# Kernel tuning notes

Hardware: AMD Instinct MI355X
Metric: run time of the kernel (lower is better)

## Reference

```python
import jax, jax.numpy as jnp
import numpy as np

# Dims: B walkers, NELEC electrons split equally into NSPIN=2 spins of NE each,
# D backflow feature dim, NION ions, SPATIAL=3 spatial dims, NORB orbitals/spin.
B, NELEC, D, NION, SPATIAL, NORB = 1024, 64, 32, 16, 3, 32
NSPIN = 2
NE = NELEC // NSPIN


def setup_inputs() -> dict:
    key = jax.random.key(0)
    ks = jax.random.split(key, 6)
    x = jax.random.normal(ks[0], (B, NELEC, D), jnp.float32)
    r_ei = jax.random.normal(ks[1], (B, NELEC, NION, SPATIAL), jnp.float32)
    # per-spin Dense(norbitals) on concatenated pair features [y_p, y_i] (2D -> NORB)
    W_orb = jax.random.normal(ks[2], (NSPIN, 2 * D, NORB), jnp.float32) / np.sqrt(2 * D)
    b_orb = jax.random.normal(ks[3], (NSPIN, NORB), jnp.float32) * 0.01
    # anisotropic decay: a 3x3 matrix per (spin, ion, orbital)
    W_env_dim = jax.random.normal(ks[4], (NSPIN, NION, SPATIAL, NORB, SPATIAL), jnp.float32) / np.sqrt(SPATIAL)
    # linear combination over ions (Dense(1), no bias)
    w_env_ion = jax.random.normal(ks[5], (NSPIN, NION), jnp.float32) / np.sqrt(NION)
    return dict(x=x, r_ei=r_ei, W_orb=W_orb, b_orb=b_orb,
                W_env_dim=W_env_dim, w_env_ion=w_env_ion)


def reference(x, r_ei, W_orb, b_orb, W_env_dim, w_env_ion):
    # Equal spin split -> stack spins as a leading axis (s = NSPIN)
    xs = jnp.stack(jnp.split(x, NSPIN, axis=-2), axis=0)       # (s, B, NE, D)
    res = jnp.stack(jnp.split(r_ei, NSPIN, axis=-3), axis=0)   # (s, B, NE, NION, 3)

    # Pairwise doubly-equivariant inputs: pair[p, i] = concat(y_p, y_i)
    xp = jnp.broadcast_to(xs[:, :, :, None, :], (NSPIN, B, NE, NE, D))
    xi = jnp.broadcast_to(xs[:, :, None, :, :], (NSPIN, B, NE, NE, D))
    pair = jnp.concatenate([xp, xi], axis=-1)                  # (s, B, NE, NE, 2D)
    orbs = jnp.einsum('sbpif,sfo->sbpio', pair, W_orb) + b_orb[:, None, None, None, :]

    # Anisotropic exponential envelope: exp(-||A_{ion,orb} (r - R_ion)||), combined over ions
    scale = jnp.einsum('sbnid,sidoe->sbnoie', res, W_env_dim)  # (s, B, NE, NORB, NION, 3)
    dist = jnp.linalg.norm(scale, axis=-1)                     # (s, B, NE, NORB, NION)
    env = jnp.einsum('sbnoi,si->sbno', jnp.exp(-dist), w_env_ion)  # (s, B, NE, NORB)

    # envelope depends on electron i (axis -2 of orbs), broadcast over p (axis -3)
    return orbs * env[:, :, None, :, :]                        # (s, B, NE, NE, NORB)
```

## Files before the change

### kernel.cpp

```cpp
#include <hip/hip_runtime.h>

#define BATCH 1024
#define NELEC 64
#define DF    32
#define NION  16
#define NORB  32
#define NE    32
#define NSB   2048
#define FACT_FLOATS (NSB * NE * NORB)
#define M_PAD 8192
#define WS_NEEDED ((size_t)(M_PAD + 3 * FACT_FLOATS) * 4)

__global__ __launch_bounds__(256) void k0_gram(
    const float* __restrict__ W_env,
    float* __restrict__ Mg)
{
    int id = blockIdx.x * 256 + threadIdx.x;
    if (id >= 2 * NION * NORB) return;
    int s = id >> 9, rem = id & 511, i = rem >> 5, o = rem & 31;
    const float* base = W_env + ((size_t)((s*NION + i) * 3) * NORB + o) * 3;
    float a0[3], a1[3], a2[3];
    #pragma unroll
    for (int e = 0; e < 3; ++e) {
        a0[e] = base[e];
        a1[e] = base[96 + e];
        a2[e] = base[192 + e];
    }
    float* out = Mg + ((size_t)(s*NION + i) * 6) * NORB + o;
    out[0*NORB] = a0[0]*a0[0] + a0[1]*a0[1] + a0[2]*a0[2];
    out[1*NORB] = a1[0]*a1[0] + a1[1]*a1[1] + a1[2]*a1[2];
    out[2*NORB] = a2[0]*a2[0] + a2[1]*a2[1] + a2[2]*a2[2];
    out[3*NORB] = 2.f*(a0[0]*a1[0] + a0[1]*a1[1] + a0[2]*a1[2]);
    out[4*NORB] = 2.f*(a0[0]*a2[0] + a0[1]*a2[1] + a0[2]*a2[2]);
    out[5*NORB] = 2.f*(a1[0]*a2[0] + a1[1]*a2[1] + a1[2]*a2[2]);
}

__global__ __launch_bounds__(256) void k1_factors(
    const float* __restrict__ x,
    const float* __restrict__ r_ei,
    const float* __restrict__ W_orb,
    const float* __restrict__ b_orb,
    const float* __restrict__ w_ion,
    const float* __restrict__ Mg,
    float* __restrict__ Uf, float* __restrict__ Ef, float* __restrict__ Wf)
{
    __shared__ float sworb[2*DF*NORB];
    __shared__ float sM[NION*6*NORB];
    __shared__ float sr[NE*52];
    __shared__ float swion[NION];

    const int t   = threadIdx.x;
    const int blk = blockIdx.x;
    const int s   = blk >> 10;
    const int b   = blk & (BATCH - 1);

    {
        const float4* g = (const float4*)(W_orb + (size_t)s * 2*DF*NORB);
        float4* d = (float4*)sworb;
        d[t] = g[t]; d[t + 256] = g[t + 256];
    }
    {
        const float4* g = (const float4*)(Mg + (size_t)s * NION*6*NORB);
        float4* d = (float4*)sM;
        d[t] = g[t]; d[t + 256] = g[t + 256]; d[t + 512] = g[t + 512];
    }
    if (t < 128) {
        const int row = t >> 2, seg = t & 3;
        const float4* g = (const float4*)(r_ei + ((size_t)b*NELEC + s*NE + row) * NION * 3);
        float4* d = (float4*)(sr + row*52 + seg*12);
        d[0] = g[seg*3 + 0]; d[1] = g[seg*3 + 1]; d[2] = g[seg*3 + 2];
    }
    if (t < NION) swion[t] = w_ion[s*NION + t];
    __syncthreads();

    const int n  = t >> 3;
    const int o0 = (t & 7) * 4;

    float u[4] = {0,0,0,0}, v[4] = {0,0,0,0};
    const float* xrow = x + ((size_t)b*NELEC + s*NE + n) * DF;
    #pragma unroll
    for (int db = 0; db < 8; ++db) {
        const float4 xa = *(const float4*)(xrow + db*4);
        #pragma unroll
        for (int k = 0; k < 4; ++k) {
            const int d = db*4 + k;
            const float4 w0 = *(const float4*)(sworb + d*NORB + o0);
            const float4 w1 = *(const float4*)(sworb + (DF + d)*NORB + o0);
            const float xk = (&xa.x)[k];
            u[0] += xk*w0.x; u[1] += xk*w0.y; u[2] += xk*w0.z; u[3] += xk*w0.w;
            v[0] += xk*w1.x; v[1] += xk*w1.y; v[2] += xk*w1.z; v[3] += xk*w1.w;
        }
    }

    float e[4] = {0,0,0,0};
    #pragma unroll
    for (int i = 0; i < NION; ++i) {
        const float r0 = sr[n*52 + i*3 + 0];
        const float r1 = sr[n*52 + i*3 + 1];
        const float r2 = sr[n*52 + i*3 + 2];
        const float q00 = r0*r0, q11 = r1*r1, q22 = r2*r2;
        const float q01 = r0*r1, q02 = r0*r2, q12 = r1*r2;
        const float* mp = sM + (size_t)(i*6) * NORB + o0;
        float d2[4];
        {
            const float4 m = *(const float4*)(mp + 0*NORB);
            d2[0] = m.x*q00; d2[1] = m.y*q00; d2[2] = m.z*q00; d2[3] = m.w*q00;
        }
        {
            const float4 m = *(const float4*)(mp + 1*NORB);
            d2[0] += m.x*q11; d2[1] += m.y*q11; d2[2] += m.z*q11; d2[3] += m.w*q11;
        }
        {
            const float4 m = *(const float4*)(mp + 2*NORB);
            d2[0] += m.x*q22; d2[1] += m.y*q22; d2[2] += m.z*q22; d2[3] += m.w*q22;
        }
        {
            const float4 m = *(const float4*)(mp + 3*NORB);
            d2[0] += m.x*q01; d2[1] += m.y*q01; d2[2] += m.z*q01; d2[3] += m.w*q01;
        }
        {
            const float4 m = *(const float4*)(mp + 4*NORB);
            d2[0] += m.x*q02; d2[1] += m.y*q02; d2[2] += m.z*q02; d2[3] += m.w*q02;
        }
        {
            const float4 m = *(const float4*)(mp + 5*NORB);
            d2[0] += m.x*q12; d2[1] += m.y*q12; d2[2] += m.z*q12; d2[3] += m.w*q12;
        }
        const float wi = swion[i];
        #pragma unroll
        for (int j = 0; j < 4; ++j) {
            const float dd = fmaxf(d2[j], 0.f);
            e[j] += wi * __expf(-sqrtf(dd));
        }
    }

    const float4 bq = *(const float4*)(b_orb + s*NORB + o0);
    const size_t wbase = (size_t)blk * (NE*NORB) + (size_t)t * 4;
    float4 uo, eo, wo;
    uo.x = u[0]; uo.y = u[1]; uo.z = u[2]; uo.w = u[3];
    eo.x = e[0]; eo.y = e[1]; eo.z = e[2]; eo.w = e[3];
    wo.x = (v[0] + bq.x) * e[0];
    wo.y = (v[1] + bq.y) * e[1];
    wo.z = (v[2] + bq.z) * e[2];
    wo.w = (v[3] + bq.w) * e[3];
    *(float4*)(Uf + wbase) = uo;
    *(float4*)(Ef + wbase) = eo;
    *(float4*)(Wf + wbase) = wo;
}

__global__ __launch_bounds__(256) void k2_expand(
    const float* __restrict__ Uf,
    const float* __restrict__ Ef,
    const float* __restrict__ Wf,
    float* __restrict__ out)
{
    __shared__ float sU[NE][NORB];
    const int t   = threadIdx.x;
    const int blk = blockIdx.x;
    const size_t base = (size_t)blk * (NE*NORB);

    ((float4*)&sU[0][0])[t] = ((const float4*)(Uf + base))[t];
    const float4 e4 = ((const float4*)(Ef + base))[t];
    const float4 w4 = ((const float4*)(Wf + base))[t];
    __syncthreads();

    const int o0 = (t & 7) * 4;
    float4* outp = (float4*)(out + (size_t)blk * (NE*NE*NORB));
    #pragma unroll
    for (int p = 0; p < NE; ++p) {
        const float4 u4 = *(const float4*)&sU[p][o0];
        float4 r;
        r.x = u4.x*e4.x + w4.x;
        r.y = u4.y*e4.y + w4.y;
        r.z = u4.z*e4.z + w4.z;
        r.w = u4.w*e4.w + w4.w;
        outp[p*256 + t] = r;
    }
}

__global__ __launch_bounds__(256) void deq_orbital_fused(
    const float* __restrict__ x, const float* __restrict__ r_ei,
    const float* __restrict__ W_orb, const float* __restrict__ b_orb,
    const float* __restrict__ W_env, const float* __restrict__ w_ion,
    float* __restrict__ out)
{
    __shared__ float sx[NE][DF];
    __shared__ float sworb[2*DF][NORB];
    __shared__ float sr[NE][NION*3];
    __shared__ float swe[NION*3*NORB*3];
    __shared__ float sU[NE][NORB];
    __shared__ float sV[NE][NORB];
    __shared__ float sE[NE][NORB];
    __shared__ float sb[NORB];
    __shared__ float swion[NION];

    const int t   = threadIdx.x;
    const int blk = blockIdx.x;
    const int s   = blk >> 10;
    const int b   = blk & (BATCH - 1);

    {
        const float4* xg = (const float4*)(x + (size_t)(b*NELEC + s*NE) * DF);
        ((float4*)&sx[0][0])[t] = xg[t];
    }
    {
        const float4* wg = (const float4*)(W_orb + (size_t)s * 2*DF*NORB);
        float4* d = (float4*)&sworb[0][0];
        d[t] = wg[t]; d[t + 256] = wg[t + 256];
    }
    {
        const float4* rg = (const float4*)(r_ei + (size_t)(b*NELEC + s*NE) * NION * 3);
        float4* d = (float4*)&sr[0][0];
        d[t] = rg[t];
        if (t < 128) d[t + 256] = rg[t + 256];
    }
    {
        const float4* weg = (const float4*)(W_env + (size_t)s * NION*3*NORB*3);
        float4* d = (float4*)swe;
        for (int j = t; j < 1152; j += 256) d[j] = weg[j];
    }
    if (t < NORB) sb[t]    = b_orb[s*NORB + t];
    if (t < NION) swion[t] = w_ion[s*NION + t];
    __syncthreads();

    const int o  = t & 31;
    const int ng = t >> 5;
    float u_acc[4], v_acc[4];
    #pragma unroll
    for (int uu = 0; uu < 4; ++uu) { u_acc[uu] = 0.f; v_acc[uu] = 0.f; }
    #pragma unroll
    for (int d = 0; d < DF; ++d) {
        const float w0 = sworb[d][o];
        const float w1 = sworb[DF + d][o];
        #pragma unroll
        for (int uu = 0; uu < 4; ++uu) {
            const float xv = sx[ng*4 + uu][d];
            u_acc[uu] += xv * w0;
            v_acc[uu] += xv * w1;
        }
    }
    #pragma unroll
    for (int uu = 0; uu < 4; ++uu) {
        sU[ng*4 + uu][o] = u_acc[uu];
        sV[ng*4 + uu][o] = v_acc[uu];
    }
    #pragma unroll
    for (int uu = 0; uu < 4; ++uu) {
        const int nn = ng*4 + uu;
        float acc = 0.f;
        #pragma unroll
        for (int i = 0; i < NION; ++i) {
            const float r0 = sr[nn][i*3 + 0];
            const float r1 = sr[nn][i*3 + 1];
            const float r2 = sr[nn][i*3 + 2];
            const float* wp = &swe[i*3*NORB*3 + o*3];
            const float s0 = r0*wp[0] + r1*wp[NORB*3    ] + r2*wp[2*NORB*3    ];
            const float s1 = r0*wp[1] + r1*wp[NORB*3 + 1] + r2*wp[2*NORB*3 + 1];
            const float s2 = r0*wp[2] + r1*wp[NORB*3 + 2] + r2*wp[2*NORB*3 + 2];
            const float dist = sqrtf(s0*s0 + s1*s1 + s2*s2);
            acc += __expf(-dist) * swion[i];
        }
        sE[nn][o] = acc;
        sV[nn][o] = (v_acc[uu] + sb[o]) * acc;
    }
    __syncthreads();

    const int io = t >> 3;
    const int o0 = (t & 7) * 4;
    const float4 e4 = *(const float4*)&sE[io][o0];
    const float4 w4 = *(const float4*)&sV[io][o0];
    float4* outp = (float4*)(out + (size_t)blk * (NE*NE*NORB));
    #pragma unroll
    for (int p = 0; p < NE; ++p) {
        const float4 u4 = *(const float4*)&sU[p][o0];
        float4 r;
        r.x = u4.x*e4.x + w4.x;
        r.y = u4.y*e4.y + w4.y;
        r.z = u4.z*e4.z + w4.z;
        r.w = u4.w*e4.w + w4.w;
        outp[p*256 + t] = r;
    }
}

extern "C" void kernel_launch(void* const* d_in, const int* in_sizes, int n_in,
                              void* d_out, int out_size, void* d_ws, size_t ws_size,
                              hipStream_t stream) {
    const float* x     = (const float*)d_in[0];
    const float* r_ei  = (const float*)d_in[1];
    const float* W_orb = (const float*)d_in[2];
    const float* b_orb = (const float*)d_in[3];
    const float* W_env = (const float*)d_in[4];
    const float* w_ion = (const float*)d_in[5];
    float* out = (float*)d_out;

    if (ws_size >= WS_NEEDED) {
        float* Mg = (float*)d_ws;
        float* Uf = Mg + M_PAD;
        float* Ef = Uf + FACT_FLOATS;
        float* Wf = Ef + FACT_FLOATS;
        k0_gram<<<4, 256, 0, stream>>>(W_env, Mg);
        k1_factors<<<NSB, 256, 0, stream>>>(x, r_ei, W_orb, b_orb, w_ion, Mg,
                                            Uf, Ef, Wf);
        k2_expand<<<NSB, 256, 0, stream>>>(Uf, Ef, Wf, out);
    } else {
        deq_orbital_fused<<<NSB, 256, 0, stream>>>(x, r_ei, W_orb, b_orb,
                                                   W_env, w_ion, out);
    }
}
```

Measured before the change: 93.22 us.

## Remap k1 threads to one orbital by four electrons and drop r_ei staging

Changes the k1_factors thread mapping from one electron by four orbitals to one orbital by four electrons. Weight and Gram-matrix reads from shared memory become scalar, conflict-free and reused across four electrons, while x and r_ei are read straight from global memory as wavefront-uniform broadcast loads. The r_ei shared staging buffer is removed. In exchange, stores become scalar rather than float4 and the r_ei loads rely on the scalar or global cache.

```diff
diff --git a/kernel.cpp b/kernel.cpp
--- a/kernel.cpp
+++ b/kernel.cpp
@@ -46,7 +46,6 @@
 {
     __shared__ float sworb[2*DF*NORB];
     __shared__ float sM[NION*6*NORB];
-    __shared__ float sr[NE*52];
     __shared__ float swion[NION];
 
     const int t   = threadIdx.x;
@@ -64,88 +63,69 @@
         float4* d = (float4*)sM;
         d[t] = g[t]; d[t + 256] = g[t + 256]; d[t + 512] = g[t + 512];
     }
-    if (t < 128) {
-        const int row = t >> 2, seg = t & 3;
-        const float4* g = (const float4*)(r_ei + ((size_t)b*NELEC + s*NE + row) * NION * 3);
-        float4* d = (float4*)(sr + row*52 + seg*12);
-        d[0] = g[seg*3 + 0]; d[1] = g[seg*3 + 1]; d[2] = g[seg*3 + 2];
-    }
     if (t < NION) swion[t] = w_ion[s*NION + t];
     __syncthreads();
 
-    const int n  = t >> 3;
-    const int o0 = (t & 7) * 4;
+    const int o  = t & 31;
+    const int ng = t >> 5;
+    const int n0 = ng * 4;
+
+    const size_t erow = (size_t)b*NELEC + s*NE + n0;
+    const float* xrow = x    + erow * DF;
+    const float* rrow = r_ei + erow * (NION*3);
 
     float u[4] = {0,0,0,0}, v[4] = {0,0,0,0};
-    const float* xrow = x + ((size_t)b*NELEC + s*NE + n) * DF;
-    #pragma unroll
+    #pragma unroll 2
     for (int db = 0; db < 8; ++db) {
-        const float4 xa = *(const float4*)(xrow + db*4);
+        float4 xa[4];
+        #pragma unroll
+        for (int e = 0; e < 4; ++e)
+            xa[e] = *(const float4*)(xrow + e*DF + db*4);
         #pragma unroll
         for (int k = 0; k < 4; ++k) {
             const int d = db*4 + k;
-            const float4 w0 = *(const float4*)(sworb + d*NORB + o0);
-            const float4 w1 = *(const float4*)(sworb + (DF + d)*NORB + o0);
-            const float xk = (&xa.x)[k];
-            u[0] += xk*w0.x; u[1] += xk*w0.y; u[2] += xk*w0.z; u[3] += xk*w0.w;
-            v[0] += xk*w1.x; v[1] += xk*w1.y; v[2] += xk*w1.z; v[3] += xk*w1.w;
-        }
-    }
-
-    float e[4] = {0,0,0,0};
-    #pragma unroll
+            const float w0 = sworb[d*NORB + o];
+            const float w1 = sworb[(DF + d)*NORB + o];
+            #pragma unroll
+            for (int e = 0; e < 4; ++e) {
+                const float xk = (&xa[e].x)[k];
+                u[e] += xk * w0;
+                v[e] += xk * w1;
+            }
+        }
+    }
+
+    float eacc[4] = {0,0,0,0};
+    #pragma unroll 4
     for (int i = 0; i < NION; ++i) {
-        const float r0 = sr[n*52 + i*3 + 0];
-        const float r1 = sr[n*52 + i*3 + 1];
-        const float r2 = sr[n*52 + i*3 + 2];
-        const float q00 = r0*r0, q11 = r1*r1, q22 = r2*r2;
-        const float q01 = r0*r1, q02 = r0*r2, q12 = r1*r2;
-        const float* mp = sM + (size_t)(i*6) * NORB + o0;
-        float d2[4];
-        {
-            const float4 m = *(const float4*)(mp + 0*NORB);
-            d2[0] = m.x*q00; d2[1] = m.y*q00; d2[2] = m.z*q00; d2[3] = m.w*q00;
-        }
-        {
-            const float4 m = *(const float4*)(mp + 1*NORB);
-            d2[0] += m.x*q11; d2[1] += m.y*q11; d2[2] += m.z*q11; d2[3] += m.w*q11;
-        }
-        {
-            const float4 m = *(const float4*)(mp + 2*NORB);
-            d2[0] += m.x*q22; d2[1] += m.y*q22; d2[2] += m.z*q22; d2[3] += m.w*q22;
-        }
-        {
-            const float4 m = *(const float4*)(mp + 3*NORB);
-            d2[0] += m.x*q01; d2[1] += m.y*q01; d2[2] += m.z*q01; d2[3] += m.w*q01;
-        }
-        {
-            const float4 m = *(const float4*)(mp + 4*NORB);
-            d2[0] += m.x*q02; d2[1] += m.y*q02; d2[2] += m.z*q02; d2[3] += m.w*q02;
-        }
-        {
-            const float4 m = *(const float4*)(mp + 5*NORB);
-            d2[0] += m.x*q12; d2[1] += m.y*q12; d2[2] += m.z*q12; d2[3] += m.w*q12;
-        }
+        const float m0 = sM[(i*6 + 0)*NORB + o];
+        const float m1 = sM[(i*6 + 1)*NORB + o];
+        const float m2 = sM[(i*6 + 2)*NORB + o];
+        const float m3 = sM[(i*6 + 3)*NORB + o];
+        const float m4 = sM[(i*6 + 4)*NORB + o];
+        const float m5 = sM[(i*6 + 5)*NORB + o];
         const float wi = swion[i];
         #pragma unroll
-        for (int j = 0; j < 4; ++j) {
-            const float dd = fmaxf(d2[j], 0.f);
-            e[j] += wi * __expf(-sqrtf(dd));
-        }
-    }
-
-    const float4 bq = *(const float4*)(b_orb + s*NORB + o0);
-    const size_t wbase = (size_t)blk * (NE*NORB) + (size_t)t * 4;
-    float4 uo, eo, wo;
-    uo.x = u[0]; uo.y = u[1]; uo.z = u[2]; uo.w = u[3];
-    eo.x = e[0]; eo.y = e[1]; eo.z = e[2]; eo.w = e[3];
-    wo.x = (v[0] + bq.x) * e[0];
-    wo.y = (v[1] + bq.y) * e[1];
-    wo.z = (v[2] + bq.z) * e[2];
-    wo.w = (v[3] + bq.w) * e[3];
-    *(float4*)(Uf + wbase) = uo;
-    *(float4*)(Ef + wbase) = eo;
-    *(float4*)(Wf + wbase) = wo;
+        for (int e = 0; e < 4; ++e) {
+            const float r0 = rrow[e*(NION*3) + i*3 + 0];
+            const float r1 = rrow[e*(NION*3) + i*3 + 1];
+            const float r2 = rrow[e*(NION*3) + i*3 + 2];
+            float d2 = m0*(r0*r0) + m1*(r1*r1) + m2*(r2*r2)
+                     + m3*(r0*r1) + m4*(r0*r2) + m5*(r1*r2);
+            d2 = fmaxf(d2, 0.f);
+            eacc[e] += wi * __expf(-sqrtf(d2));
+        }
+    }
+
+    const float bo = b_orb[s*NORB + o];
+    const size_t base = (size_t)blk * (NE*NORB);
+    #pragma unroll
+    for (int e = 0; e < 4; ++e) {
+        const int idx = (n0 + e)*NORB + o;
+        Uf[base + idx] = u[e];
+        Ef[base + idx] = eacc[e];
+        Wf[base + idx] = (v[e] + bo) * eacc[e];
+    }
 }
 
 __global__ __launch_bounds__(256) void k2_expand(
```

Measured after the change: 107.9 us. 1.16x slower.
